# Kernel optimization log

Hardware: AMD Instinct MI355X
Metric: run time of the kernel (lower is better)

The kernel has to match this reference:

```python
import jax, jax.numpy as jnp
import numpy as np

K = 11          # kernel_size
SIGMA = 1.5
CH = 3          # image channels


def _gaussian_kernel(ch):
    coords = jnp.arange(K, dtype=jnp.float32) - (K - 1) / 2
    g = jnp.exp(-coords ** 2 / (2 * SIGMA ** 2))
    g = g / g.sum()
    k2d = jnp.outer(g, g)                       # [K, K]
    return jnp.tile(k2d[None, None], (ch, 1, 1, 1))  # [C, 1, K, K] depthwise


def setup_inputs() -> dict:
    key = jax.random.key(0)
    kx, ky = jax.random.split(key)
    x = jax.random.normal(kx, (32, CH, 512, 512), dtype=jnp.float32)
    y = jax.random.normal(ky, (32, CH, 512, 512), dtype=jnp.float32)
    kernel = _gaussian_kernel(CH)
    return {"x": x, "y": y, "kernel": kernel}


def _blur(v, kernel):
    # depthwise 2D Gaussian blur, SAME padding (K odd)
    c = v.shape[1]
    pad = K // 2
    return jax.lax.conv_general_dilated(
        v, kernel, window_strides=(1, 1), padding=[(pad, pad), (pad, pad)],
        dimension_numbers=("NCHW", "OIHW", "NCHW"), feature_group_count=c)


def reference(x, y, kernel):
    C1 = 0.01 ** 2
    C2 = 0.03 ** 2
    mu_x = _blur(x, kernel)
    mu_y = _blur(y, kernel)
    sigma_x = _blur(x * x, kernel) - mu_x ** 2
    sigma_y = _blur(y * y, kernel) - mu_y ** 2
    sigma_xy = _blur(x * y, kernel) - mu_x * mu_y
    ssim_num = (2 * mu_x * mu_y + C1) * (2 * sigma_xy + C2)
    ssim_den = (mu_x ** 2 + mu_y ** 2 + C1) * (sigma_x + sigma_y + C2)
    ssim = ssim_num / (ssim_den + 1e-8)
    return ((1.0 - ssim) / 2.0).mean()
```

## Files before the change

### kernel.cpp

```cpp
#include <hip/hip_runtime.h>
#include <hip/hip_bf16.h>

#define IMG    512
#define KSZ    11
#define HALO   5
#define STRIP  64
#define PANEL  16
#define RSTR32 330
#define FOFF   66

typedef short bf16x8 __attribute__((ext_vector_type(8)));
typedef float f32x4  __attribute__((ext_vector_type(4)));
union S8 { bf16x8 v; ushort u16[8]; uint u32[4]; };

__device__ __forceinline__ uint cvtpk(float lo, float hi) {
    uint r;
    asm("v_cvt_pk_bf16_f32 %0, %1, %2" : "=v"(r) : "v"(lo), "v"(hi));
    return r;
}
__device__ __forceinline__ float2 pk_mul(float2 a, float2 b) {
    float2 d;
    asm("v_pk_mul_f32 %0, %1, %2" : "=v"(d) : "v"(a), "v"(b));
    return d;
}
__device__ __forceinline__ ushort f2bf(float f) {
    union { __hip_bfloat16 h; ushort u; } c;
    c.h = __float2bfloat16(f);
    return c.u;
}


__global__ __launch_bounds__(256)
void dssim_mfma_kernel(const float* __restrict__ x,
                       const float* __restrict__ y,
                       const float* __restrict__ kern,
                       float* __restrict__ out)
{
    __shared__ float  sgf[16];
    __shared__ ushort gext[64];
    __shared__ uint   Ring32[24 * RSTR32];
    __shared__ float  wsum[4];

    const int tid = threadIdx.x;
    const int l   = tid & 63;
    const int wv  = tid >> 6;
    const int q   = l >> 4;
    const int cj  = l & 15;
    const int wcb = wv * 16 + cj;

    if (tid < KSZ) {
        float s = 0.f;
        #pragma unroll
        for (int j = 0; j < KSZ; ++j) s += kern[tid * KSZ + j];
        sgf[tid] = s;
    }
    for (int i = tid; i < 3 * RSTR32; i += 256) Ring32[i] = 0u;
    __syncthreads();
    if (tid < 64) {
        const int d = tid - 18;
        gext[tid] = (d >= 0 && d < KSZ) ? f2bf(sgf[d]) : (ushort)0;
    }
    __syncthreads();

    S8 tgh, tgv;
    #pragma unroll
    for (int ii = 0; ii < 8; ++ii) {
        tgh.u16[ii] = gext[15 + q * 8 + ii - cj];
        tgv.u16[ii] = gext[17 + q * 8 + ii - cj];
    }

    const int plane  = blockIdx.z;
    const int half   = blockIdx.y;
    const int cstrip = blockIdx.x * STRIP;
    const int base   = plane * (IMG * IMG);

    const int  cb    = cstrip - 8 + 16 * wv + 8 * q;
    const bool colok = (cb >= 0) && (cb + 8 <= IMG);
    const float* xp  = x + base + cb;
    const float* yp  = y + base + cb;

    const int t0   = half ? 15 : 0;
    const int t1   = half ? 32 : 16;
    const int vmin = half ? 17 : 1;

    f32x4 xa, xb, ya, yb;
    auto load8 = [&](int t) {
        const int r = t * PANEL + cj;
        if (r < IMG && colok) {
            const float* px = xp + r * IMG;
            const float* py = yp + r * IMG;
            xa = *(const f32x4*)px;  xb = *(const f32x4*)(px + 4);
            ya = *(const f32x4*)py;  yb = *(const f32x4*)(py + 4);
        } else {
            const f32x4 zz = {0.f, 0.f, 0.f, 0.f};
            xa = zz; xb = zz; ya = zz; yb = zz;
        }
    };

    load8(t0);

    const f32x4 z0 = {0.f, 0.f, 0.f, 0.f};
    const float C1 = 1e-4f, C2 = 9e-4f;
    float local = 0.f;
    int hb = (8 * t0) % 24;

    for (int t = t0; t <= t1; ++t) {
        float2 x01 = {xa[0], xa[1]}, x23 = {xa[2], xa[3]};
        float2 x45 = {xb[0], xb[1]}, x67 = {xb[2], xb[3]};
        float2 y01 = {ya[0], ya[1]}, y23 = {ya[2], ya[3]};
        float2 y45 = {yb[0], yb[1]}, y67 = {yb[2], yb[3]};
        S8 fx, fy, fxx, fyy, fxy;
        #pragma unroll
        for (int w = 0; w < 4; ++w) {
            const float2 xv = (w == 0) ? x01 : (w == 1) ? x23 : (w == 2) ? x45 : x67;
            const float2 yv = (w == 0) ? y01 : (w == 1) ? y23 : (w == 2) ? y45 : y67;
            const float2 xxv = pk_mul(xv, xv);
            const float2 yyv = pk_mul(yv, yv);
            const float2 xyv = pk_mul(xv, yv);
            fx .u32[w] = cvtpk(xv.x,  xv.y);
            fy .u32[w] = cvtpk(yv.x,  yv.y);
            fxx.u32[w] = cvtpk(xxv.x, xxv.y);
            fyy.u32[w] = cvtpk(yyv.x, yyv.y);
            fxy.u32[w] = cvtpk(xyv.x, xyv.y);
        }

        if (t < t1) load8(t + 1);

        {
            int p0 = hb + 2 * q + 3;  if (p0 >= 24) p0 -= 24;
            int p1 = p0 + 1;          if (p1 >= 24) p1 -= 24;
            const int rw0 = p0 * RSTR32 + wcb;
            const int rw1 = p1 * RSTR32 + wcb;
            f32x4 d;
            d = __builtin_amdgcn_mfma_f32_16x16x32_bf16(fx.v,  tgh.v, z0, 0, 0, 0);
            Ring32[rw0 + 0 * FOFF] = cvtpk(d[0], d[1]);
            Ring32[rw1 + 0 * FOFF] = cvtpk(d[2], d[3]);
            d = __builtin_amdgcn_mfma_f32_16x16x32_bf16(fy.v,  tgh.v, z0, 0, 0, 0);
            Ring32[rw0 + 1 * FOFF] = cvtpk(d[0], d[1]);
            Ring32[rw1 + 1 * FOFF] = cvtpk(d[2], d[3]);
            d = __builtin_amdgcn_mfma_f32_16x16x32_bf16(fxx.v, tgh.v, z0, 0, 0, 0);
            Ring32[rw0 + 2 * FOFF] = cvtpk(d[0], d[1]);
            Ring32[rw1 + 2 * FOFF] = cvtpk(d[2], d[3]);
            d = __builtin_amdgcn_mfma_f32_16x16x32_bf16(fyy.v, tgh.v, z0, 0, 0, 0);
            Ring32[rw0 + 3 * FOFF] = cvtpk(d[0], d[1]);
            Ring32[rw1 + 3 * FOFF] = cvtpk(d[2], d[3]);
            d = __builtin_amdgcn_mfma_f32_16x16x32_bf16(fxy.v, tgh.v, z0, 0, 0, 0);
            Ring32[rw0 + 4 * FOFF] = cvtpk(d[0], d[1]);
            Ring32[rw1 + 4 * FOFF] = cvtpk(d[2], d[3]);
        }

        __syncthreads();

        if (t >= vmin) {
            const int vb = (hb >= 8) ? hb - 8 : hb + 16;
            int vr[4];
            #pragma unroll
            for (int ii = 0; ii < 4; ++ii) {
                int pp = vb + 4 * q + ii;  if (pp >= 24) pp -= 24;
                vr[ii] = pp * RSTR32 + wcb;
            }
            f32x4 vf[5];
            #pragma unroll
            for (int f = 0; f < 5; ++f) {
                S8 b;
                #pragma unroll
                for (int ii = 0; ii < 4; ++ii) b.u32[ii] = Ring32[vr[ii] + f * FOFF];
                vf[f] = __builtin_amdgcn_mfma_f32_16x16x32_bf16(tgv.v, b.v, z0, 0, 0, 0);
            }
            #pragma unroll
            for (int r = 0; r < 4; ++r) {
                const float mx  = vf[0][r], my  = vf[1][r];
                const float exx = vf[2][r], eyy = vf[3][r], exy = vf[4][r];
                const float sxv = fmaf(-mx, mx, exx);
                const float syv = fmaf(-my, my, eyy);
                const float sxy = fmaf(-mx, my, exy);
                const float num = fmaf(2.f, mx * my, C1) * fmaf(2.f, sxy, C2);
                const float den = fmaf(mx, mx, fmaf(my, my, C1)) * (sxv + syv + C2);
                const float ssim = __fdividef(num, den + 1e-8f);
                local += (1.f - ssim) * 0.5f;
            }
        }

        __syncthreads();

        hb += 8;  if (hb >= 24) hb -= 24;
    }

    #pragma unroll
    for (int o = 32; o > 0; o >>= 1) local += __shfl_down(local, o, 64);
    if (l == 0) wsum[wv] = local;
    __syncthreads();
    if (tid == 0) {
        const float s = wsum[0] + wsum[1] + wsum[2] + wsum[3];
        atomicAdd(out, s * (1.f / 25165824.f));
    }
}

extern "C" void kernel_launch(void* const* d_in, const int* in_sizes, int n_in,
                              void* d_out, int out_size, void* d_ws, size_t ws_size,
                              hipStream_t stream)
{
    const float* x    = (const float*)d_in[0];
    const float* y    = (const float*)d_in[1];
    const float* kern = (const float*)d_in[2];
    float* out = (float*)d_out;

    hipMemsetAsync(out, 0, sizeof(float), stream);

    dim3 grid(IMG / STRIP, 2, 32 * 3);
    dssim_mfma_kernel<<<grid, 256, 0, stream>>>(x, y, kern, out);
}
```

Baseline: 81.38 us.

## Give each wave a private LDS ring and drop per-step block barriers

The shared LDS ring used for horizontal-to-vertical blur exchange is split into one private region per wavefront, laid out so each wave only reads columns it wrote itself. This lets both __syncthreads per row panel be removed, since there is no longer any cross-wave data dependence, and waves can run out of lockstep. It relies on the assumption that intra-wave LDS writes are visible to later reads in the same wave without an explicit barrier. It also changes the padding and stride layout, which can alter bank-conflict behaviour.

```diff
diff --git a/kernel.cpp b/kernel.cpp
--- a/kernel.cpp
+++ b/kernel.cpp
@@ -6,8 +6,8 @@
 #define HALO   5
 #define STRIP  64
 #define PANEL  16
-#define RSTR32 330
-#define FOFF   66
+#define WPS    84
+#define WRSZ   (24 * WPS)
 
 typedef short bf16x8 __attribute__((ext_vector_type(8)));
 typedef float f32x4  __attribute__((ext_vector_type(4)));
@@ -38,7 +38,7 @@
 {
     __shared__ float  sgf[16];
     __shared__ ushort gext[64];
-    __shared__ uint   Ring32[24 * RSTR32];
+    __shared__ uint   Wring[4 * WRSZ];
     __shared__ float  wsum[4];
 
     const int tid = threadIdx.x;
@@ -46,7 +46,7 @@
     const int wv  = tid >> 6;
     const int q   = l >> 4;
     const int cj  = l & 15;
-    const int wcb = wv * 16 + cj;
+    const int wb  = wv * WRSZ;
 
     if (tid < KSZ) {
         float s = 0.f;
@@ -54,7 +54,7 @@
         for (int j = 0; j < KSZ; ++j) s += kern[tid * KSZ + j];
         sgf[tid] = s;
     }
-    for (int i = tid; i < 3 * RSTR32; i += 256) Ring32[i] = 0u;
+    for (int i = l; i < 3 * WPS; i += 64) Wring[wb + i] = 0u;
     __syncthreads();
     if (tid < 64) {
         const int d = tid - 18;
@@ -129,27 +129,25 @@
         {
             int p0 = hb + 2 * q + 3;  if (p0 >= 24) p0 -= 24;
             int p1 = p0 + 1;          if (p1 >= 24) p1 -= 24;
-            const int rw0 = p0 * RSTR32 + wcb;
-            const int rw1 = p1 * RSTR32 + wcb;
+            const int rw0 = wb + p0 * WPS + cj;
+            const int rw1 = wb + p1 * WPS + cj;
             f32x4 d;
             d = __builtin_amdgcn_mfma_f32_16x16x32_bf16(fx.v,  tgh.v, z0, 0, 0, 0);
-            Ring32[rw0 + 0 * FOFF] = cvtpk(d[0], d[1]);
-            Ring32[rw1 + 0 * FOFF] = cvtpk(d[2], d[3]);
+            Wring[rw0 +  0] = cvtpk(d[0], d[1]);
+            Wring[rw1 +  0] = cvtpk(d[2], d[3]);
             d = __builtin_amdgcn_mfma_f32_16x16x32_bf16(fy.v,  tgh.v, z0, 0, 0, 0);
-            Ring32[rw0 + 1 * FOFF] = cvtpk(d[0], d[1]);
-            Ring32[rw1 + 1 * FOFF] = cvtpk(d[2], d[3]);
+            Wring[rw0 + 16] = cvtpk(d[0], d[1]);
+            Wring[rw1 + 16] = cvtpk(d[2], d[3]);
             d = __builtin_amdgcn_mfma_f32_16x16x32_bf16(fxx.v, tgh.v, z0, 0, 0, 0);
-            Ring32[rw0 + 2 * FOFF] = cvtpk(d[0], d[1]);
-            Ring32[rw1 + 2 * FOFF] = cvtpk(d[2], d[3]);
+            Wring[rw0 + 32] = cvtpk(d[0], d[1]);
+            Wring[rw1 + 32] = cvtpk(d[2], d[3]);
             d = __builtin_amdgcn_mfma_f32_16x16x32_bf16(fyy.v, tgh.v, z0, 0, 0, 0);
-            Ring32[rw0 + 3 * FOFF] = cvtpk(d[0], d[1]);
-            Ring32[rw1 + 3 * FOFF] = cvtpk(d[2], d[3]);
+            Wring[rw0 + 48] = cvtpk(d[0], d[1]);
+            Wring[rw1 + 48] = cvtpk(d[2], d[3]);
             d = __builtin_amdgcn_mfma_f32_16x16x32_bf16(fxy.v, tgh.v, z0, 0, 0, 0);
-            Ring32[rw0 + 4 * FOFF] = cvtpk(d[0], d[1]);
-            Ring32[rw1 + 4 * FOFF] = cvtpk(d[2], d[3]);
-        }
-
-        __syncthreads();
+            Wring[rw0 + 64] = cvtpk(d[0], d[1]);
+            Wring[rw1 + 64] = cvtpk(d[2], d[3]);
+        }
 
         if (t >= vmin) {
             const int vb = (hb >= 8) ? hb - 8 : hb + 16;
@@ -157,14 +155,14 @@
             #pragma unroll
             for (int ii = 0; ii < 4; ++ii) {
                 int pp = vb + 4 * q + ii;  if (pp >= 24) pp -= 24;
-                vr[ii] = pp * RSTR32 + wcb;
+                vr[ii] = wb + pp * WPS + cj;
             }
             f32x4 vf[5];
             #pragma unroll
             for (int f = 0; f < 5; ++f) {
                 S8 b;
                 #pragma unroll
-                for (int ii = 0; ii < 4; ++ii) b.u32[ii] = Ring32[vr[ii] + f * FOFF];
+                for (int ii = 0; ii < 4; ++ii) b.u32[ii] = Wring[vr[ii] + f * 16];
                 vf[f] = __builtin_amdgcn_mfma_f32_16x16x32_bf16(tgv.v, b.v, z0, 0, 0, 0);
             }
             #pragma unroll
@@ -181,8 +179,6 @@
             }
         }
 
-        __syncthreads();
-
         hb += 8;  if (hb >= 24) hb -= 24;
     }
 
```

New measurement: 82.97 us. Within noise of the previous version (+2.0%).
